# Optimization experiments

Hardware: AMD Instinct MI355X
Metric: run time of the kernel (lower is better)

Reference implementation:

```python
import jax, jax.numpy as jnp
import numpy as np

B, H, HKV, S, D = 1, 32, 4, 2048, 128
NEG = -1e9  # causal mask fill (float32-safe, like torch finfo.min in spirit)


def setup_inputs() -> dict:
    key = jax.random.key(0)
    kq, kk, kv, ks = jax.random.split(key, 4)
    query = jax.random.normal(kq, (B, H, S, D), dtype=jnp.float32)
    k = jax.random.normal(kk, (B, HKV, S, D), dtype=jnp.float32)
    v = jax.random.normal(kv, (B, HKV, S, D), dtype=jnp.float32)
    sinks = jax.random.normal(ks, (H,), dtype=jnp.float32)
    # causal additive mask [B, 1, S, S]
    causal = jnp.where(jnp.tril(jnp.ones((S, S), dtype=bool)), 0.0, NEG).astype(jnp.float32)
    attention_mask = jnp.broadcast_to(causal[None, None], (B, 1, S, S))
    return {"query": query, "key": k, "value": v,
            "attention_mask": attention_mask, "sinks": sinks}


def reference(query, key, value, attention_mask, sinks):
    scaling = 1.0 / jnp.sqrt(jnp.asarray(D, dtype=query.dtype))
    groups = H // HKV
    # repeat_kv: [B, HKV, S, D] -> [B, H, S, D]
    k = jnp.repeat(key, groups, axis=1)
    v = jnp.repeat(value, groups, axis=1)
    # scores [B, H, S, S]
    attn = jnp.einsum('bhqd,bhkd->bhqk', query, k) * scaling
    attn = attn + attention_mask[:, :, :, :attn.shape[-1]]
    # append per-head sink column -> [B, H, S, S+1]
    sink_col = jnp.broadcast_to(sinks.reshape(1, H, 1, 1), (B, H, S, 1)).astype(attn.dtype)
    combined = jnp.concatenate([attn, sink_col], axis=-1)
    combined = combined - jnp.max(combined, axis=-1, keepdims=True)
    probs = jax.nn.softmax(combined, axis=-1)[..., :-1]
    # PV matmul, then [B, H, S, D] -> [B, S, H, D]
    out = jnp.einsum('bhqk,bhkd->bhqd', probs, v)
    return jnp.transpose(out, (0, 2, 1, 3))
```

## Files before the change

### kernel.cpp

```cpp
#include <hip/hip_runtime.h>
#include <hip/hip_bf16.h>

#define NH   32
#define SEQ  2048
#define HD   128
#define QBLK 64
#define KVB  64
#define NQT  (SEQ / QBLK)
#define NUNITS (NQT * NH)
#define TILE_ELEMS (KVB * HD)
#define TILE_BYTES 16384

typedef __attribute__((ext_vector_type(8))) short bf16x8;
typedef __attribute__((ext_vector_type(4))) float f32x4;
typedef __attribute__((ext_vector_type(2))) unsigned int u32x2;

#define VMCNT0 asm volatile("s_waitcnt vmcnt(0)" ::: "memory")

static __device__ __forceinline__ unsigned short f2bf(float f) {
  __hip_bfloat16 h = __float2bfloat16(f);
  union { __hip_bfloat16 h; unsigned short u; } c; c.h = h;
  return c.u;
}

__device__ __forceinline__ int swzK(int row, int colByte) {
  return row * 256 + (colByte ^ ((row & 7) << 4));
}
__device__ __forceinline__ int swzV(int d, int kvByte) {
  return d * 128 + (kvByte ^ ((d & 7) << 4));
}
__device__ __forceinline__ int swzP(int row, int colByte) {
  return row * 128 + (colByte ^ ((row & 7) << 4));
}

__global__ __launch_bounds__(256)
void convert_kv(const float* __restrict__ K, const float* __restrict__ V,
                unsigned short* __restrict__ Ki, unsigned short* __restrict__ Vi)
{
  const int b = blockIdx.x;
  const float* Ks = K + (size_t)b * TILE_ELEMS;
  const float* Vs = V + (size_t)b * TILE_ELEMS;
  char* ki = (char*)(Ki + (size_t)b * TILE_ELEMS);
  char* vi = (char*)(Vi + (size_t)b * TILE_ELEMS);
  const int tid  = threadIdx.x;
  const int srow = tid >> 4;
  const int scol = (tid & 15) * 8;
  #pragma unroll
  for (int i = 0; i < 4; ++i) {
    const int row = i * 16 + srow;
    float tk[8], tv[8];
    *(f32x4*)(tk)     = *(const f32x4*)(Ks + row * HD + scol);
    *(f32x4*)(tk + 4) = *(const f32x4*)(Ks + row * HD + scol + 4);
    *(f32x4*)(tv)     = *(const f32x4*)(Vs + row * HD + scol);
    *(f32x4*)(tv + 4) = *(const f32x4*)(Vs + row * HD + scol + 4);
    bf16x8 k8;
    #pragma unroll
    for (int j = 0; j < 8; ++j) k8[j] = (short)f2bf(tk[j]);
    *(bf16x8*)(ki + swzK(row, scol * 2)) = k8;
    #pragma unroll
    for (int j = 0; j < 8; ++j)
      *(unsigned short*)(vi + swzV(scol + j, row * 2)) = f2bf(tv[j]);
  }
}

__device__ __forceinline__ void stage_tile(const unsigned short* img, char* lds, int tid) {
  #pragma unroll
  for (int k = 0; k < 4; ++k)
    __builtin_amdgcn_global_load_lds((const unsigned int*)((const char*)img + k * 4096 + tid * 16),
                                     (unsigned int*)(lds + k * 4096 + tid * 16), 16, 0, 0);
}

__global__ __launch_bounds__(256, 4)
void attn_fwd(const float* __restrict__ Q, const float* __restrict__ sinks,
              const unsigned short* __restrict__ Kimg, const unsigned short* __restrict__ Vimg,
              float* __restrict__ out, int* __restrict__ counter)
{
  __shared__ __align__(16) char Kl[2][TILE_BYTES];
  __shared__ __align__(16) char Vl[2][TILE_BYTES];
  __shared__ __align__(16) char Pl[4][2048];
  __shared__ int sh_unit;

  const int tid  = threadIdx.x;
  const int lane = tid & 63;
  const int w    = tid >> 6;
  const int lr   = lane & 15;
  const int lg   = lane >> 4;

  const float QSC = 0.08838834764831845f * 1.4426950408889634f;
  const float EC  = 17.312340490667562f;

  bf16x8 ones;
  #pragma unroll
  for (int i = 0; i < 8; ++i) ones[i] = (short)0x3F80;
  char* pw = Pl[w];

  for (;;) {
    if (tid == 0) sh_unit = atomicAdd(counter, 1);
    __syncthreads();
    const int u = sh_unit;
    if (u >= NUNITS) break;

    const int qt  = (NQT - 1) - (u >> 5);
    const int h   = u & 31;
    const int kvh = h >> 3;
    const int q0  = qt * QBLK;
    const int nt  = qt + 1;

    const unsigned short* Kt = Kimg + (size_t)(kvh * 32) * TILE_ELEMS;
    const unsigned short* Vt = Vimg + (size_t)(kvh * 32) * TILE_ELEMS;

    stage_tile(Kt, Kl[0], tid);
    stage_tile(Vt, Vl[0], tid);

    const int qb   = q0 + w * 16;
    const int qmax = qb + 15;
    const int qme  = qb + lr;

    bf16x8 qa[4];
    {
      const float* qp = Q + (size_t)(h * SEQ + qb + lr) * HD + lg * 8;
      #pragma unroll
      for (int ks = 0; ks < 4; ++ks) {
        float t0[8];
        *(f32x4*)(t0)     = *(const f32x4*)(qp + ks * 32);
        *(f32x4*)(t0 + 4) = *(const f32x4*)(qp + ks * 32 + 4);
        bf16x8 qv;
        #pragma unroll
        for (int jj = 0; jj < 8; ++jj) qv[jj] = (short)f2bf(t0[jj] * QSC);
        qa[ks] = qv;
      }
    }

    f32x4 acc[8];
    f32x4 accl = (f32x4){0.f, 0.f, 0.f, 0.f};
    #pragma unroll
    for (int i = 0; i < 8; ++i) acc[i] = (f32x4){0.f, 0.f, 0.f, 0.f};

    for (int i = 0; i < nt; ++i) {
      VMCNT0;
      __syncthreads();
      if (i + 1 < nt) {
        stage_tile(Kt + (size_t)(i + 1) * TILE_ELEMS, Kl[(i + 1) & 1], tid);
        stage_tile(Vt + (size_t)(i + 1) * TILE_ELEMS, Vl[(i + 1) & 1], tid);
      }

      const int kv0 = i * KVB;
      if (kv0 > qmax) continue;
      const char* kb = Kl[i & 1];
      const char* vb = Vl[i & 1];

      f32x4 sc[4];
      __builtin_amdgcn_s_setprio(1);
      #pragma unroll
      for (int cb = 0; cb < 4; ++cb) {
        f32x4 a = (f32x4){0.f, 0.f, 0.f, 0.f};
        #pragma unroll
        for (int ks = 0; ks < 4; ++ks) {
          bf16x8 kf = *(const bf16x8*)(kb + swzK(cb * 16 + lr, (ks * 32 + lg * 8) * 2));
          a = __builtin_amdgcn_mfma_f32_16x16x32_bf16(kf, qa[ks], a, 0, 0, 0);
        }
        sc[cb] = a;
      }
      __builtin_amdgcn_s_setprio(0);

      #pragma unroll
      for (int cb = 0; cb < 4; ++cb) {
        float p[4];
        #pragma unroll
        for (int r = 0; r < 4; ++r) {
          const int kv = kv0 + cb * 16 + lg * 4 + r;
          float e = __builtin_amdgcn_exp2f(sc[cb][r] - EC);
          p[r] = (kv > qme) ? 0.f : e;
        }
        u32x2 wd;
        wd[0] = (unsigned int)f2bf(p[0]) | ((unsigned int)f2bf(p[1]) << 16);
        wd[1] = (unsigned int)f2bf(p[2]) | ((unsigned int)f2bf(p[3]) << 16);
        *(u32x2*)(pw + swzP(lr, cb * 32 + lg * 8)) = wd;
      }

      bf16x8 pa[2];
      #pragma unroll
      for (int h2 = 0; h2 < 2; ++h2)
        pa[h2] = *(const bf16x8*)(pw + swzP(lr, h2 * 64 + lg * 16));

      accl = __builtin_amdgcn_mfma_f32_16x16x32_bf16(pa[0], ones, accl, 0, 0, 0);
      accl = __builtin_amdgcn_mfma_f32_16x16x32_bf16(pa[1], ones, accl, 0, 0, 0);
      __builtin_amdgcn_s_setprio(1);
      #pragma unroll
      for (int ncb = 0; ncb < 8; ++ncb) {
        bf16x8 vf0 = *(const bf16x8*)(vb + swzV(ncb * 16 + lr, lg * 16));
        bf16x8 vf1 = *(const bf16x8*)(vb + swzV(ncb * 16 + lr, 64 + lg * 16));
        acc[ncb] = __builtin_amdgcn_mfma_f32_16x16x32_bf16(pa[0], vf0, acc[ncb], 0, 0, 0);
        acc[ncb] = __builtin_amdgcn_mfma_f32_16x16x32_bf16(pa[1], vf1, acc[ncb], 0, 0, 0);
      }
      __builtin_amdgcn_s_setprio(0);
    }

    const float sk = sinks[h];
    const float sadd = __builtin_amdgcn_exp2f(sk * 1.4426950408889634f - EC);
    #pragma unroll
    for (int r = 0; r < 4; ++r) {
      const float rd = 1.0f / (accl[r] + sadd);
      const size_t q = qb + lg * 4 + r;
      float* op = out + (q * NH + h) * HD + lr;
      #pragma unroll
      for (int ncb = 0; ncb < 8; ++ncb)
        op[ncb * 16] = acc[ncb][r] * rd;
    }
  }
}

extern "C" void kernel_launch(void* const* d_in, const int* in_sizes, int n_in,
                              void* d_out, int out_size, void* d_ws, size_t ws_size,
                              hipStream_t stream) {
  const float* Q     = (const float*)d_in[0];
  const float* K     = (const float*)d_in[1];
  const float* V     = (const float*)d_in[2];
  const float* sinks = (const float*)d_in[4];
  float* out = (float*)d_out;

  unsigned short* Kimg = (unsigned short*)d_ws;
  unsigned short* Vimg = Kimg + (size_t)128 * TILE_ELEMS;
  int* counter = (int*)((char*)d_ws + (size_t)8 * 1024 * 1024 / 2);

  hipMemsetAsync(counter, 0, 64, stream);
  convert_kv<<<dim3(128), 256, 0, stream>>>(K, V, Kimg, Vimg);
  attn_fwd<<<dim3(512), 256, 0, stream>>>(Q, sinks, Kimg, Vimg, out, counter);
}
```

Before: 86.32 us.

## Replace atomic work queue with static balanced grid and 32-wide KV tiles

Drops the persistent atomic-counter scheduler and its memset, and launches one block per (q-tile, head) unit. A fixed interleaved mapping assigns long and short causal q-tiles across block ranges to balance load. The KV tile shrinks from 64 to 32 rows, halving LDS use per buffer so more blocks can be resident per CU. The trade-off is twice as many loop iterations and barriers, and more staging overhead per unit of work.

```diff
diff --git a/kernel.cpp b/kernel.cpp
--- a/kernel.cpp
+++ b/kernel.cpp
@@ -4,12 +4,9 @@
 #define NH   32
 #define SEQ  2048
 #define HD   128
-#define QBLK 64
-#define KVB  64
-#define NQT  (SEQ / QBLK)
-#define NUNITS (NQT * NH)
+#define KVB  32
 #define TILE_ELEMS (KVB * HD)
-#define TILE_BYTES 16384
+#define TILE_BYTES 8192
 
 typedef __attribute__((ext_vector_type(8))) short bf16x8;
 typedef __attribute__((ext_vector_type(4))) float f32x4;
@@ -26,27 +23,27 @@
 __device__ __forceinline__ int swzK(int row, int colByte) {
   return row * 256 + (colByte ^ ((row & 7) << 4));
 }
-__device__ __forceinline__ int swzV(int d, int kvByte) {
-  return d * 128 + (kvByte ^ ((d & 7) << 4));
-}
-__device__ __forceinline__ int swzP(int row, int colByte) {
-  return row * 128 + (colByte ^ ((row & 7) << 4));
+__device__ __forceinline__ int swzV32(int d, int kvByte) {
+  return d * 64 + (kvByte ^ ((d & 3) << 4));
+}
+__device__ __forceinline__ int swzP32(int row, int colByte) {
+  return row * 64 + (colByte ^ ((row & 3) << 4));
 }
 
 __global__ __launch_bounds__(256)
 void convert_kv(const float* __restrict__ K, const float* __restrict__ V,
-                unsigned short* __restrict__ Ki, unsigned short* __restrict__ Vi)
+                char* __restrict__ Ki, char* __restrict__ Vi)
 {
   const int b = blockIdx.x;
   const float* Ks = K + (size_t)b * TILE_ELEMS;
   const float* Vs = V + (size_t)b * TILE_ELEMS;
-  char* ki = (char*)(Ki + (size_t)b * TILE_ELEMS);
-  char* vi = (char*)(Vi + (size_t)b * TILE_ELEMS);
+  char* kt = Ki + (size_t)b * TILE_BYTES;
+  char* vt = Vi + (size_t)b * TILE_BYTES;
   const int tid  = threadIdx.x;
   const int srow = tid >> 4;
   const int scol = (tid & 15) * 8;
   #pragma unroll
-  for (int i = 0; i < 4; ++i) {
+  for (int i = 0; i < 2; ++i) {
     const int row = i * 16 + srow;
     float tk[8], tv[8];
     *(f32x4*)(tk)     = *(const f32x4*)(Ks + row * HD + scol);
@@ -56,29 +53,33 @@
     bf16x8 k8;
     #pragma unroll
     for (int j = 0; j < 8; ++j) k8[j] = (short)f2bf(tk[j]);
-    *(bf16x8*)(ki + swzK(row, scol * 2)) = k8;
+    *(bf16x8*)(kt + swzK(row, scol * 2)) = k8;
     #pragma unroll
     for (int j = 0; j < 8; ++j)
-      *(unsigned short*)(vi + swzV(scol + j, row * 2)) = f2bf(tv[j]);
-  }
-}
-
-__device__ __forceinline__ void stage_tile(const unsigned short* img, char* lds, int tid) {
-  #pragma unroll
-  for (int k = 0; k < 4; ++k)
-    __builtin_amdgcn_global_load_lds((const unsigned int*)((const char*)img + k * 4096 + tid * 16),
-                                     (unsigned int*)(lds + k * 4096 + tid * 16), 16, 0, 0);
+      *(unsigned short*)(vt + swzV32(scol + j, row * 2)) = f2bf(tv[j]);
+  }
+}
+
+__device__ __forceinline__ void stage_tile(const char* kimg, const char* vimg,
+                                           char* kb, char* vb, int tid) {
+  #pragma unroll
+  for (int k = 0; k < 2; ++k)
+    __builtin_amdgcn_global_load_lds((const unsigned int*)(kimg + k * 4096 + tid * 16),
+                                     (unsigned int*)(kb + k * 4096 + tid * 16), 16, 0, 0);
+  #pragma unroll
+  for (int k = 0; k < 2; ++k)
+    __builtin_amdgcn_global_load_lds((const unsigned int*)(vimg + k * 4096 + tid * 16),
+                                     (unsigned int*)(vb + k * 4096 + tid * 16), 16, 0, 0);
 }
 
 __global__ __launch_bounds__(256, 4)
 void attn_fwd(const float* __restrict__ Q, const float* __restrict__ sinks,
-              const unsigned short* __restrict__ Kimg, const unsigned short* __restrict__ Vimg,
-              float* __restrict__ out, int* __restrict__ counter)
+              const char* __restrict__ Ki, const char* __restrict__ Vi,
+              float* __restrict__ out)
 {
   __shared__ __align__(16) char Kl[2][TILE_BYTES];
   __shared__ __align__(16) char Vl[2][TILE_BYTES];
-  __shared__ __align__(16) char Pl[4][2048];
-  __shared__ int sh_unit;
+  __shared__ __align__(16) char Pl[4][1024];
 
   const int tid  = threadIdx.x;
   const int lane = tid & 63;
@@ -86,127 +87,120 @@
   const int lr   = lane & 15;
   const int lg   = lane >> 4;
 
+  const int bid = blockIdx.x;
+  const int s   = bid >> 8;
+  const int a   = bid & 255;
+  const int h   = a & 31;
+  const int r8  = a >> 5;
+  int qt;
+  if      (s == 0) qt = 31 - r8;
+  else if (s == 1) qt = r8;
+  else if (s == 2) qt = 23 - r8;
+  else             qt = 8 + r8;
+  const int q0  = qt * 64;
+  const int nt  = (qt + 1) * 2;
+  const int kvh = h >> 3;
+
+  const char* Kt = Ki + (size_t)(kvh * 64) * TILE_BYTES;
+  const char* Vt = Vi + (size_t)(kvh * 64) * TILE_BYTES;
+
+  stage_tile(Kt, Vt, Kl[0], Vl[0], tid);
+
   const float QSC = 0.08838834764831845f * 1.4426950408889634f;
   const float EC  = 17.312340490667562f;
 
+  const int qb   = q0 + w * 16;
+  const int qmax = qb + 15;
+  const int qme  = qb + lr;
+
+  bf16x8 qa[4];
+  {
+    const float* qp = Q + (size_t)(h * SEQ + qme) * HD + lg * 8;
+    #pragma unroll
+    for (int ks = 0; ks < 4; ++ks) {
+      float t0[8];
+      *(f32x4*)(t0)     = *(const f32x4*)(qp + ks * 32);
+      *(f32x4*)(t0 + 4) = *(const f32x4*)(qp + ks * 32 + 4);
+      bf16x8 qv;
+      #pragma unroll
+      for (int jj = 0; jj < 8; ++jj) qv[jj] = (short)f2bf(t0[jj] * QSC);
+      qa[ks] = qv;
+    }
+  }
+
+  f32x4 acc[8];
+  f32x4 accl = (f32x4){0.f, 0.f, 0.f, 0.f};
+  #pragma unroll
+  for (int i = 0; i < 8; ++i) acc[i] = (f32x4){0.f, 0.f, 0.f, 0.f};
   bf16x8 ones;
   #pragma unroll
   for (int i = 0; i < 8; ++i) ones[i] = (short)0x3F80;
   char* pw = Pl[w];
 
-  for (;;) {
-    if (tid == 0) sh_unit = atomicAdd(counter, 1);
+  for (int i = 0; i < nt; ++i) {
+    VMCNT0;
     __syncthreads();
-    const int u = sh_unit;
-    if (u >= NUNITS) break;
-
-    const int qt  = (NQT - 1) - (u >> 5);
-    const int h   = u & 31;
-    const int kvh = h >> 3;
-    const int q0  = qt * QBLK;
-    const int nt  = qt + 1;
-
-    const unsigned short* Kt = Kimg + (size_t)(kvh * 32) * TILE_ELEMS;
-    const unsigned short* Vt = Vimg + (size_t)(kvh * 32) * TILE_ELEMS;
-
-    stage_tile(Kt, Kl[0], tid);
-    stage_tile(Vt, Vl[0], tid);
-
-    const int qb   = q0 + w * 16;
-    const int qmax = qb + 15;
-    const int qme  = qb + lr;
-
-    bf16x8 qa[4];
-    {
-      const float* qp = Q + (size_t)(h * SEQ + qb + lr) * HD + lg * 8;
+    if (i + 1 < nt)
+      stage_tile(Kt + (size_t)(i + 1) * TILE_BYTES,
+                 Vt + (size_t)(i + 1) * TILE_BYTES,
+                 Kl[(i + 1) & 1], Vl[(i + 1) & 1], tid);
+
+    const int kv0 = i * KVB;
+    if (kv0 > qmax) continue;
+    const char* kb = Kl[i & 1];
+    const char* vb = Vl[i & 1];
+
+    f32x4 sc[2];
+    __builtin_amdgcn_s_setprio(1);
+    #pragma unroll
+    for (int cb = 0; cb < 2; ++cb) {
+      f32x4 a2 = (f32x4){0.f, 0.f, 0.f, 0.f};
       #pragma unroll
       for (int ks = 0; ks < 4; ++ks) {
-        float t0[8];
-        *(f32x4*)(t0)     = *(const f32x4*)(qp + ks * 32);
-        *(f32x4*)(t0 + 4) = *(const f32x4*)(qp + ks * 32 + 4);
-        bf16x8 qv;
-        #pragma unroll
-        for (int jj = 0; jj < 8; ++jj) qv[jj] = (short)f2bf(t0[jj] * QSC);
-        qa[ks] = qv;
+        bf16x8 kf = *(const bf16x8*)(kb + swzK(cb * 16 + lr, (ks * 32 + lg * 8) * 2));
+        a2 = __builtin_amdgcn_mfma_f32_16x16x32_bf16(kf, qa[ks], a2, 0, 0, 0);
       }
-    }
-
-    f32x4 acc[8];
-    f32x4 accl = (f32x4){0.f, 0.f, 0.f, 0.f};
-    #pragma unroll
-    for (int i = 0; i < 8; ++i) acc[i] = (f32x4){0.f, 0.f, 0.f, 0.f};
-
-    for (int i = 0; i < nt; ++i) {
-      VMCNT0;
-      __syncthreads();
-      if (i + 1 < nt) {
-        stage_tile(Kt + (size_t)(i + 1) * TILE_ELEMS, Kl[(i + 1) & 1], tid);
-        stage_tile(Vt + (size_t)(i + 1) * TILE_ELEMS, Vl[(i + 1) & 1], tid);
+      sc[cb] = a2;
+    }
+    __builtin_amdgcn_s_setprio(0);
+
+    #pragma unroll
+    for (int cb = 0; cb < 2; ++cb) {
+      float p[4];
+      #pragma unroll
+      for (int r = 0; r < 4; ++r) {
+        const int kv = kv0 + cb * 16 + lg * 4 + r;
+        float e = __builtin_amdgcn_exp2f(sc[cb][r] - EC);
+        p[r] = (kv > qme) ? 0.f : e;
       }
-
-      const int kv0 = i * KVB;
-      if (kv0 > qmax) continue;
-      const char* kb = Kl[i & 1];
-      const char* vb = Vl[i & 1];
-
-      f32x4 sc[4];
-      __builtin_amdgcn_s_setprio(1);
-      #pragma unroll
-      for (int cb = 0; cb < 4; ++cb) {
-        f32x4 a = (f32x4){0.f, 0.f, 0.f, 0.f};
-        #pragma unroll
-        for (int ks = 0; ks < 4; ++ks) {
-          bf16x8 kf = *(const bf16x8*)(kb + swzK(cb * 16 + lr, (ks * 32 + lg * 8) * 2));
-          a = __builtin_amdgcn_mfma_f32_16x16x32_bf16(kf, qa[ks], a, 0, 0, 0);
-        }
-        sc[cb] = a;
-      }
-      __builtin_amdgcn_s_setprio(0);
-
-      #pragma unroll
-      for (int cb = 0; cb < 4; ++cb) {
-        float p[4];
-        #pragma unroll
-        for (int r = 0; r < 4; ++r) {
-          const int kv = kv0 + cb * 16 + lg * 4 + r;
-          float e = __builtin_amdgcn_exp2f(sc[cb][r] - EC);
-          p[r] = (kv > qme) ? 0.f : e;
-        }
-        u32x2 wd;
-        wd[0] = (unsigned int)f2bf(p[0]) | ((unsigned int)f2bf(p[1]) << 16);
-        wd[1] = (unsigned int)f2bf(p[2]) | ((unsigned int)f2bf(p[3]) << 16);
-        *(u32x2*)(pw + swzP(lr, cb * 32 + lg * 8)) = wd;
-      }
-
-      bf16x8 pa[2];
-      #pragma unroll
-      for (int h2 = 0; h2 < 2; ++h2)
-        pa[h2] = *(const bf16x8*)(pw + swzP(lr, h2 * 64 + lg * 16));
-
-      accl = __builtin_amdgcn_mfma_f32_16x16x32_bf16(pa[0], ones, accl, 0, 0, 0);
-      accl = __builtin_amdgcn_mfma_f32_16x16x32_bf16(pa[1], ones, accl, 0, 0, 0);
-      __builtin_amdgcn_s_setprio(1);
-      #pragma unroll
-      for (int ncb = 0; ncb < 8; ++ncb) {
-        bf16x8 vf0 = *(const bf16x8*)(vb + swzV(ncb * 16 + lr, lg * 16));
-        bf16x8 vf1 = *(const bf16x8*)(vb + swzV(ncb * 16 + lr, 64 + lg * 16));
-        acc[ncb] = __builtin_amdgcn_mfma_f32_16x16x32_bf16(pa[0], vf0, acc[ncb], 0, 0, 0);
-        acc[ncb] = __builtin_amdgcn_mfma_f32_16x16x32_bf16(pa[1], vf1, acc[ncb], 0, 0, 0);
-      }
-      __builtin_amdgcn_s_setprio(0);
-    }
-
-    const float sk = sinks[h];
-    const float sadd = __builtin_amdgcn_exp2f(sk * 1.4426950408889634f - EC);
-    #pragma unroll
-    for (int r = 0; r < 4; ++r) {
-      const float rd = 1.0f / (accl[r] + sadd);
-      const size_t q = qb + lg * 4 + r;
-      float* op = out + (q * NH + h) * HD + lr;
-      #pragma unroll
-      for (int ncb = 0; ncb < 8; ++ncb)
-        op[ncb * 16] = acc[ncb][r] * rd;
-    }
+      u32x2 wd;
+      wd[0] = (unsigned int)f2bf(p[0]) | ((unsigned int)f2bf(p[1]) << 16);
+      wd[1] = (unsigned int)f2bf(p[2]) | ((unsigned int)f2bf(p[3]) << 16);
+      *(u32x2*)(pw + swzP32(lr, cb * 32 + lg * 8)) = wd;
+    }
+
+    bf16x8 pa = *(const bf16x8*)(pw + swzP32(lr, lg * 16));
+
+    accl = __builtin_amdgcn_mfma_f32_16x16x32_bf16(pa, ones, accl, 0, 0, 0);
+    __builtin_amdgcn_s_setprio(1);
+    #pragma unroll
+    for (int ncb = 0; ncb < 8; ++ncb) {
+      bf16x8 vf = *(const bf16x8*)(vb + swzV32(ncb * 16 + lr, lg * 16));
+      acc[ncb] = __builtin_amdgcn_mfma_f32_16x16x32_bf16(pa, vf, acc[ncb], 0, 0, 0);
+    }
+    __builtin_amdgcn_s_setprio(0);
+  }
+
+  const float sk = sinks[h];
+  const float sadd = __builtin_amdgcn_exp2f(sk * 1.4426950408889634f - EC);
+  #pragma unroll
+  for (int r = 0; r < 4; ++r) {
+    const float rd = 1.0f / (accl[r] + sadd);
+    const size_t q = qb + lg * 4 + r;
+    float* op = out + (q * NH + h) * HD + lr;
+    #pragma unroll
+    for (int ncb = 0; ncb < 8; ++ncb)
+      op[ncb * 16] = acc[ncb][r] * rd;
   }
 }
 
@@ -219,11 +213,9 @@
   const float* sinks = (const float*)d_in[4];
   float* out = (float*)d_out;
 
-  unsigned short* Kimg = (unsigned short*)d_ws;
-  unsigned short* Vimg = Kimg + (size_t)128 * TILE_ELEMS;
-  int* counter = (int*)((char*)d_ws + (size_t)8 * 1024 * 1024 / 2);
-
-  hipMemsetAsync(counter, 0, 64, stream);
-  convert_kv<<<dim3(128), 256, 0, stream>>>(K, V, Kimg, Vimg);
-  attn_fwd<<<dim3(512), 256, 0, stream>>>(Q, sinks, Kimg, Vimg, out, counter);
-}
+  char* Ki = (char*)d_ws;
+  char* Vi = Ki + (size_t)256 * TILE_BYTES;
+
+  convert_kv<<<dim3(256), 256, 0, stream>>>(K, V, Ki, Vi);
+  attn_fwd<<<dim3(1024), 256, 0, stream>>>(Q, sinks, Ki, Vi, out);
+}
```

After: 82.84 us. 4.0% less time.
